# Kernel optimization log

Hardware: AMD Instinct MI355X
Metric: run time of the kernel (lower is better)

Reference implementation:

```python
import jax, jax.numpy as jnp
import numpy as np

N = 1048576
HID = 64
GEO = 15


def _glorot(key, in_dim, out_dim):
    # torch nn.Linear default init: U(-1/sqrt(in), 1/sqrt(in)); stored here as [in, out]
    bound = 1.0 / np.sqrt(in_dim)
    return jax.random.uniform(key, (in_dim, out_dim), jnp.float32, -bound, bound)


def setup_inputs() -> dict:
    key = jax.random.key(0)
    ks = jax.random.split(key, 8)
    x = jax.random.normal(ks[0], (N, 6), dtype=jnp.float32)
    # sigma_net: 3 -> 64 -> 64 -> (1 + geo_feat_dim)=16, no bias
    ws0 = _glorot(ks[1], 3, HID)
    ws1 = _glorot(ks[2], HID, HID)
    ws2 = _glorot(ks[3], HID, 1 + GEO)
    # color_net: (3 + 15)=18 -> 64 -> 64 -> 3, no bias
    wc0 = _glorot(ks[4], 3 + GEO, HID)
    wc1 = _glorot(ks[5], HID, HID)
    wc2 = _glorot(ks[6], HID, HID)
    wc3 = _glorot(ks[7], HID, 3)
    return {"x": x, "ws0": ws0, "ws1": ws1, "ws2": ws2,
            "wc0": wc0, "wc1": wc1, "wc2": wc2, "wc3": wc3}


def reference(x, ws0, ws1, ws2, wc0, wc1, wc2, wc3):
    input_pts, input_views = x[..., :3], x[..., 3:]
    # sigma net: Linear+ReLU x2, final Linear
    h = jax.nn.relu(input_pts @ ws0)
    h = jax.nn.relu(h @ ws1)
    h = h @ ws2                       # [N, 16]
    sigma = jax.nn.softplus(h[..., 0])  # [N]
    geo_feat = h[..., 1:]               # [N, 15]
    # color net
    c = jnp.concatenate([input_views, geo_feat], axis=-1)  # [N, 18]
    c = jax.nn.relu(c @ wc0)
    c = jax.nn.relu(c @ wc1)
    c = jax.nn.relu(c @ wc2)
    color = c @ wc3                    # [N, 3]
    return jnp.concatenate([color, sigma[..., None]], axis=-1)  # [N, 4]
```

## Files before the change

### kernel.cpp

```cpp
#include <hip/hip_runtime.h>
#include <math.h>
#include <stdint.h>

typedef short bf16x8 __attribute__((ext_vector_type(8)));
typedef float f32x4 __attribute__((ext_vector_type(4)));

#define NFRAGS 36
#define T 3
#define NW 4
#define BS 256
#define PTS_BLK (NW * T * 16)

__device__ __forceinline__ uint32_t f2bf_rne(float f) {
    uint32_t u = __float_as_uint(f);
    return (u + 0x7FFFu + ((u >> 16) & 1u)) >> 16;
}

__device__ __forceinline__ uint32_t pk2(float a, float b) {
    return __builtin_amdgcn_perm(__float_as_uint(b), __float_as_uint(a), 0x07060302u);
}
__device__ __forceinline__ uint32_t relu2(uint32_t x) {
    uint32_t r;
    asm("v_pk_max_i16 %0, %1, 0" : "=v"(r) : "v"(x));
    return r;
}
__device__ __forceinline__ uint32_t pk2r(float a, float b) { return relu2(pk2(a, b)); }
__device__ __forceinline__ uint16_t bfu(float v) { return (uint16_t)(__float_as_uint(v) >> 16); }

__device__ __forceinline__ int sperm(int k) {
    return (k & 3) | (((k >> 2) & 3) << 4) | (((k >> 4) & 3) << 2);
}
__device__ __forceinline__ int rperm(int k) {
    return (k & 32) | (((k >> 3) & 1) << 4) | (((k >> 4) & 1) << 3) | (k & 7);
}

__global__ void pack_weights(const float* __restrict__ ws0, const float* __restrict__ ws1,
                             const float* __restrict__ ws2, const float* __restrict__ wc0,
                             const float* __restrict__ wc1, const float* __restrict__ wc2,
                             const float* __restrict__ wc3, uint4* __restrict__ wpack) {
    int idx = blockIdx.x * blockDim.x + threadIdx.x;
    if (idx >= NFRAGS * 64) return;
    int F = idx >> 6, cl = idx & 63, cm = cl & 15, cq = cl >> 4;
    const float* w; int IN, OUT, mt, ks, pm;
    if (F < 4)       { w = ws0; IN = 3;  OUT = 64; mt = F;            ks = 0;          pm = 0; }
    else if (F < 12) { w = ws1; IN = 64; OUT = 64; mt = (F-4) >> 1;   ks = (F-4) & 1;  pm = 2; }
    else if (F < 14) { w = ws2; IN = 64; OUT = 16; mt = 0;            ks = F - 12;     pm = 2; }
    else if (F < 18) { w = wc0; IN = 18; OUT = 64; mt = F - 14;       ks = 0;          pm = 0; }
    else if (F < 26) { w = wc1; IN = 64; OUT = 64; mt = (F-18) >> 1;  ks = (F-18) & 1; pm = 2; }
    else if (F < 34) { w = wc2; IN = 64; OUT = 64; mt = (F-26) >> 1;  ks = (F-26) & 1; pm = 2; }
    else             { w = wc3; IN = 64; OUT = 3;  mt = 0;            ks = F - 34;     pm = 2; }
    const int fo = mt * 16 + cm;
    uint32_t pk[4];
    for (int jj = 0; jj < 4; ++jj) {
        uint32_t h[2];
        for (int bb = 0; bb < 2; ++bb) {
            int kg = ks * 32 + cq * 8 + jj * 2 + bb;
            int kr = (pm == 2) ? sperm(rperm(kg)) : kg;
            float v = 0.f;
            if (fo < OUT && kr < IN) v = w[kr * OUT + fo];
            h[bb] = f2bf_rne(v);
        }
        pk[jj] = h[0] | (h[1] << 16);
    }
    wpack[F * 64 + cl] = make_uint4(pk[0], pk[1], pk[2], pk[3]);
}

__global__ __launch_bounds__(BS, 4) void nerf_main(const float* __restrict__ xin,
                                                   const uint4* __restrict__ wpack,
                                                   float* __restrict__ outp, int n) {
    __shared__ __align__(16) char smem[NW * T * 2048];
    const int tid = threadIdx.x, wv = tid >> 6, lane = tid & 63;
    const int p = lane & 15, q = lane >> 4;
    const int sw = p & 7;
    char* actw = smem + wv * (T * 2048);
    const int base = blockIdx.x * PTS_BLK + wv * (T * 16);

    auto aaddr = [&](int t, int g) -> char* {
        return actw + t * 2048 + p * 128 + ((g ^ sw) << 4);
    };
    auto ldA = [&](int F) -> bf16x8 {
        uint4 u = wpack[F * 64 + lane];
        return *(bf16x8*)&u;
    };
    const f32x4 z4 = {0.f, 0.f, 0.f, 0.f};

    auto xpose = [&](const f32x4* d, bf16x8& b0, bf16x8& b1) {
        uint32_t X0 = pk2r(d[0][0], d[0][1]), X1 = pk2r(d[0][2], d[0][3]);
        uint32_t X2 = pk2r(d[1][0], d[1][1]), X3 = pk2r(d[1][2], d[1][3]);
        uint32_t X4 = pk2r(d[2][0], d[2][1]), X5 = pk2r(d[2][2], d[2][3]);
        uint32_t X6 = pk2r(d[3][0], d[3][1]), X7 = pk2r(d[3][2], d[3][3]);
        asm("v_permlane32_swap_b32 %0, %1" : "+v"(X0), "+v"(X4));
        asm("v_permlane32_swap_b32 %0, %1" : "+v"(X1), "+v"(X5));
        asm("v_permlane32_swap_b32 %0, %1" : "+v"(X2), "+v"(X6));
        asm("v_permlane32_swap_b32 %0, %1" : "+v"(X3), "+v"(X7));
        uint4 u0 = make_uint4(X0, X1, X2, X3), u1 = make_uint4(X4, X5, X6, X7);
        b0 = *(bf16x8*)&u0; b1 = *(bf16x8*)&u1;
    };

    float x0 = 0.f, x1 = 0.f, x2 = 0.f;
    float vv0 = 0.f, vv1 = 0.f, vv2 = 0.f;
    {
        const int pi = base + q * 16 + p;
        if (q < T && pi < n) {
            const float2* xp = (const float2*)(xin + (size_t)pi * 6);
            float2 a = xp[0], b = xp[1], c = xp[2];
            x0 = a.x; x1 = a.y; x2 = b.x; vv0 = b.y; vv1 = c.x; vv2 = c.y;
        }
    }

    bf16x8 W0[4];
#pragma unroll
    for (int i = 0; i < 4; ++i) W0[i] = ldA(i);
    bf16x8 W1[8];
#pragma unroll
    for (int i = 0; i < 8; ++i) W1[i] = ldA(4 + i);

    if (q < T) {
        *(uint4*)aaddr(q, 0) = make_uint4(pk2(x0, x1), pk2(x2, 0.f), 0u, 0u);
        *(uint4*)aaddr(q, 1) = make_uint4(0u, 0u, 0u, 0u);
        *(uint4*)aaddr(q, 2) = make_uint4(0u, 0u, 0u, 0u);
        *(uint4*)aaddr(q, 3) = make_uint4(0u, 0u, 0u, 0u);
    }

    bf16x8 c0[T], c1[T];

    auto layerK32 = [&](const bf16x8 (&W)[4]) {
#pragma unroll
        for (int t = 0; t < T; ++t) {
            bf16x8 b = *(const bf16x8*)aaddr(t, q);
            f32x4 d[4];
#pragma unroll
            for (int mt = 0; mt < 4; ++mt)
                d[mt] = __builtin_amdgcn_mfma_f32_16x16x32_bf16(W[mt], b, z4, 0, 0, 0);
            xpose(d, c0[t], c1[t]);
        }
    };

    auto layer64 = [&](const bf16x8 (&W)[8]) {
#pragma unroll
        for (int t = 0; t < T; ++t) {
            f32x4 d[4];
#pragma unroll
            for (int mt = 0; mt < 4; ++mt) {
                f32x4 acc = __builtin_amdgcn_mfma_f32_16x16x32_bf16(W[mt*2],   c0[t], z4,  0, 0, 0);
                d[mt]     = __builtin_amdgcn_mfma_f32_16x16x32_bf16(W[mt*2+1], c1[t], acc, 0, 0, 0);
            }
            xpose(d, c0[t], c1[t]);
        }
    };

    layerK32(W0);

    bf16x8 W2[2];
    W2[0] = ldA(12); W2[1] = ldA(13);

    layer64(W1);

    bf16x8 W3[4];
#pragma unroll
    for (int i = 0; i < 4; ++i) W3[i] = ldA(14 + i);

    float sig[T];
    {
#pragma unroll
        for (int t = 0; t < T; ++t) {
            f32x4 acc = __builtin_amdgcn_mfma_f32_16x16x32_bf16(W2[0], c0[t], z4,  0, 0, 0);
            f32x4 d   = __builtin_amdgcn_mfma_f32_16x16x32_bf16(W2[1], c1[t], acc, 0, 0, 0);
            const float sx = d[0];
            sig[t] = fmaxf(sx, 0.f) + __logf(1.f + __expf(-fabsf(sx)));
            *(uint4*)aaddr(t, q) = make_uint4(0u, 0u, 0u, 0u);
            if (q == t) {
                *(uint32_t*)(aaddr(t, 0) + 0) = pk2(vv0, vv1);
                *(uint16_t*)(aaddr(t, 0) + 4) = bfu(vv2);
            }
            if (q == 0) {
                *(uint16_t*)(aaddr(t, 0) + 6) = bfu(d[1]);
                *(uint32_t*)(aaddr(t, 0) + 8) = pk2(d[2], d[3]);
            } else if (q == 1) {
                *(uint32_t*)(aaddr(t, 0) + 12) = pk2(d[0], d[1]);
                *(uint32_t*)(aaddr(t, 1) + 0)  = pk2(d[2], d[3]);
            } else if (q == 2) {
                *(uint32_t*)(aaddr(t, 1) + 4) = pk2(d[0], d[1]);
                *(uint32_t*)(aaddr(t, 1) + 8) = pk2(d[2], d[3]);
            } else {
                *(uint32_t*)(aaddr(t, 1) + 12) = pk2(d[0], d[1]);
                *(uint32_t*)(aaddr(t, 2) + 0)  = pk2(d[2], d[3]);
            }
        }
    }

    bf16x8 W4[8];
#pragma unroll
    for (int i = 0; i < 8; ++i) W4[i] = ldA(18 + i);

    layerK32(W3);

    bf16x8 W5[8];
#pragma unroll
    for (int i = 0; i < 8; ++i) W5[i] = ldA(26 + i);

    layer64(W4);

    bf16x8 W6[2];
    W6[0] = ldA(34); W6[1] = ldA(35);

    layer64(W5);

    {
#pragma unroll
        for (int t = 0; t < T; ++t) {
            f32x4 acc = __builtin_amdgcn_mfma_f32_16x16x32_bf16(W6[0], c0[t], z4,  0, 0, 0);
            f32x4 d   = __builtin_amdgcn_mfma_f32_16x16x32_bf16(W6[1], c1[t], acc, 0, 0, 0);
            if (q == 0) {
                const int pt = base + t * 16 + p;
                if (pt < n)
                    *(float4*)(outp + (size_t)pt * 4) = make_float4(d[0], d[1], d[2], sig[t]);
            }
        }
    }
}

extern "C" void kernel_launch(void* const* d_in, const int* in_sizes, int n_in,
                              void* d_out, int out_size, void* d_ws, size_t ws_size,
                              hipStream_t stream) {
    const float* x   = (const float*)d_in[0];
    const float* ws0 = (const float*)d_in[1];
    const float* ws1 = (const float*)d_in[2];
    const float* ws2 = (const float*)d_in[3];
    const float* wc0 = (const float*)d_in[4];
    const float* wc1 = (const float*)d_in[5];
    const float* wc2 = (const float*)d_in[6];
    const float* wc3 = (const float*)d_in[7];
    float* out = (float*)d_out;
    uint4* wpack = (uint4*)d_ws;

    const int n = in_sizes[0] / 6;
    pack_weights<<<(NFRAGS * 64 + 255) / 256, 256, 0, stream>>>(ws0, ws1, ws2, wc0, wc1, wc2, wc3, wpack);
    const int grid = (n + PTS_BLK - 1) / PTS_BLK;
    nerf_main<<<grid, BS, 0, stream>>>(x, wpack, out, n);
}
```

Measured before the change: 116.1 us.

## Use persistent blocks with LDS-resident weights and prefetch of next chunk inputs

Measured after the change: 125.4 us. 8.0% more time.

```diff
diff --git a/kernel.cpp b/kernel.cpp
--- a/kernel.cpp
+++ b/kernel.cpp
@@ -6,10 +6,13 @@
 typedef float f32x4 __attribute__((ext_vector_type(4)));
 
 #define NFRAGS 36
-#define T 3
+#define T 4
 #define NW 4
 #define BS 256
 #define PTS_BLK (NW * T * 16)
+#define WBYTES (NFRAGS * 1024)
+#define ABYTES (NW * T * 1024)
+#define GRID_P 768
 
 __device__ __forceinline__ uint32_t f2bf_rne(float f) {
     uint32_t u = __float_as_uint(f);
@@ -67,20 +70,28 @@
 
 __global__ __launch_bounds__(BS, 4) void nerf_main(const float* __restrict__ xin,
                                                    const uint4* __restrict__ wpack,
-                                                   float* __restrict__ outp, int n) {
-    __shared__ __align__(16) char smem[NW * T * 2048];
+                                                   float* __restrict__ outp,
+                                                   int n, int nchunks) {
+    __shared__ __align__(16) char smem[WBYTES + ABYTES];
     const int tid = threadIdx.x, wv = tid >> 6, lane = tid & 63;
     const int p = lane & 15, q = lane >> 4;
-    const int sw = p & 7;
-    char* actw = smem + wv * (T * 2048);
-    const int base = blockIdx.x * PTS_BLK + wv * (T * 16);
-
+
+    {
+        uint4* wl = (uint4*)smem;
+        const uint4* __restrict__ ws = wpack;
+#pragma unroll
+        for (int i = 0; i < (NFRAGS * 64) / BS; ++i)
+            wl[tid + i * BS] = ws[tid + i * BS];
+    }
+
+    char* wbase = smem + lane * 16;
+    auto ldW = [&](int F) -> bf16x8 {
+        return *(const bf16x8*)(wbase + F * 1024);
+    };
+
+    char* actp = smem + WBYTES + wv * (T * 1024) + p * 64;
     auto aaddr = [&](int t, int g) -> char* {
-        return actw + t * 2048 + p * 128 + ((g ^ sw) << 4);
-    };
-    auto ldA = [&](int F) -> bf16x8 {
-        uint4 u = wpack[F * 64 + lane];
-        return *(bf16x8*)&u;
+        return actp + t * 1024 + (((g ^ (p & 3))) << 4);
     };
     const f32x4 z4 = {0.f, 0.f, 0.f, 0.f};
 
@@ -97,126 +108,123 @@
         b0 = *(bf16x8*)&u0; b1 = *(bf16x8*)&u1;
     };
 
-    float x0 = 0.f, x1 = 0.f, x2 = 0.f;
-    float vv0 = 0.f, vv1 = 0.f, vv2 = 0.f;
-    {
-        const int pi = base + q * 16 + p;
-        if (q < T && pi < n) {
+    bf16x8 c0[T], c1[T];
+
+    auto layerK32 = [&](int FB) {
+        bf16x8 W0 = ldW(FB), W1 = ldW(FB + 1), W2 = ldW(FB + 2), W3 = ldW(FB + 3);
+#pragma unroll
+        for (int t = 0; t < T; ++t) {
+            bf16x8 b = *(const bf16x8*)aaddr(t, q);
+            f32x4 d[4];
+            d[0] = __builtin_amdgcn_mfma_f32_16x16x32_bf16(W0, b, z4, 0, 0, 0);
+            d[1] = __builtin_amdgcn_mfma_f32_16x16x32_bf16(W1, b, z4, 0, 0, 0);
+            d[2] = __builtin_amdgcn_mfma_f32_16x16x32_bf16(W2, b, z4, 0, 0, 0);
+            d[3] = __builtin_amdgcn_mfma_f32_16x16x32_bf16(W3, b, z4, 0, 0, 0);
+            xpose(d, c0[t], c1[t]);
+        }
+    };
+
+    auto layer64 = [&](int FB) {
+        bf16x8 W[8];
+#pragma unroll
+        for (int i = 0; i < 8; ++i) W[i] = ldW(FB + i);
+#pragma unroll
+        for (int t = 0; t < T; ++t) {
+            f32x4 d[4];
+#pragma unroll
+            for (int mt = 0; mt < 4; ++mt) {
+                f32x4 acc = __builtin_amdgcn_mfma_f32_16x16x32_bf16(W[mt*2],   c0[t], z4,  0, 0, 0);
+                d[mt]     = __builtin_amdgcn_mfma_f32_16x16x32_bf16(W[mt*2+1], c1[t], acc, 0, 0, 0);
+            }
+            xpose(d, c0[t], c1[t]);
+        }
+    };
+
+    int chunk = blockIdx.x;
+    float2 xa = {0.f, 0.f}, xb = {0.f, 0.f}, xc = {0.f, 0.f};
+    if (chunk < nchunks) {
+        const int pi = chunk * PTS_BLK + wv * (T * 16) + q * 16 + p;
+        if (pi < n) {
             const float2* xp = (const float2*)(xin + (size_t)pi * 6);
-            float2 a = xp[0], b = xp[1], c = xp[2];
-            x0 = a.x; x1 = a.y; x2 = b.x; vv0 = b.y; vv1 = c.x; vv2 = c.y;
-        }
-    }
-
-    bf16x8 W0[4];
-#pragma unroll
-    for (int i = 0; i < 4; ++i) W0[i] = ldA(i);
-    bf16x8 W1[8];
-#pragma unroll
-    for (int i = 0; i < 8; ++i) W1[i] = ldA(4 + i);
-
-    if (q < T) {
-        *(uint4*)aaddr(q, 0) = make_uint4(pk2(x0, x1), pk2(x2, 0.f), 0u, 0u);
+            xa = xp[0]; xb = xp[1]; xc = xp[2];
+        }
+    }
+
+    __syncthreads();
+
+    for (; chunk < nchunks; chunk += gridDim.x) {
+        const int base = chunk * PTS_BLK + wv * (T * 16);
+        const float vv0 = xb.y, vv1 = xc.x, vv2 = xc.y;
+
+        *(uint4*)aaddr(q, 0) = make_uint4(pk2(xa.x, xa.y), pk2(xb.x, 0.f), 0u, 0u);
         *(uint4*)aaddr(q, 1) = make_uint4(0u, 0u, 0u, 0u);
         *(uint4*)aaddr(q, 2) = make_uint4(0u, 0u, 0u, 0u);
         *(uint4*)aaddr(q, 3) = make_uint4(0u, 0u, 0u, 0u);
-    }
-
-    bf16x8 c0[T], c1[T];
-
-    auto layerK32 = [&](const bf16x8 (&W)[4]) {
-#pragma unroll
-        for (int t = 0; t < T; ++t) {
-            bf16x8 b = *(const bf16x8*)aaddr(t, q);
-            f32x4 d[4];
-#pragma unroll
-            for (int mt = 0; mt < 4; ++mt)
-                d[mt] = __builtin_amdgcn_mfma_f32_16x16x32_bf16(W[mt], b, z4, 0, 0, 0);
-            xpose(d, c0[t], c1[t]);
-        }
-    };
-
-    auto layer64 = [&](const bf16x8 (&W)[8]) {
-#pragma unroll
-        for (int t = 0; t < T; ++t) {
-            f32x4 d[4];
-#pragma unroll
-            for (int mt = 0; mt < 4; ++mt) {
-                f32x4 acc = __builtin_amdgcn_mfma_f32_16x16x32_bf16(W[mt*2],   c0[t], z4,  0, 0, 0);
-                d[mt]     = __builtin_amdgcn_mfma_f32_16x16x32_bf16(W[mt*2+1], c1[t], acc, 0, 0, 0);
-            }
-            xpose(d, c0[t], c1[t]);
-        }
-    };
-
-    layerK32(W0);
-
-    bf16x8 W2[2];
-    W2[0] = ldA(12); W2[1] = ldA(13);
-
-    layer64(W1);
-
-    bf16x8 W3[4];
-#pragma unroll
-    for (int i = 0; i < 4; ++i) W3[i] = ldA(14 + i);
-
-    float sig[T];
-    {
-#pragma unroll
-        for (int t = 0; t < T; ++t) {
-            f32x4 acc = __builtin_amdgcn_mfma_f32_16x16x32_bf16(W2[0], c0[t], z4,  0, 0, 0);
-            f32x4 d   = __builtin_amdgcn_mfma_f32_16x16x32_bf16(W2[1], c1[t], acc, 0, 0, 0);
-            const float sx = d[0];
-            sig[t] = fmaxf(sx, 0.f) + __logf(1.f + __expf(-fabsf(sx)));
-            *(uint4*)aaddr(t, q) = make_uint4(0u, 0u, 0u, 0u);
-            if (q == t) {
-                *(uint32_t*)(aaddr(t, 0) + 0) = pk2(vv0, vv1);
-                *(uint16_t*)(aaddr(t, 0) + 4) = bfu(vv2);
-            }
-            if (q == 0) {
-                *(uint16_t*)(aaddr(t, 0) + 6) = bfu(d[1]);
-                *(uint32_t*)(aaddr(t, 0) + 8) = pk2(d[2], d[3]);
-            } else if (q == 1) {
-                *(uint32_t*)(aaddr(t, 0) + 12) = pk2(d[0], d[1]);
-                *(uint32_t*)(aaddr(t, 1) + 0)  = pk2(d[2], d[3]);
-            } else if (q == 2) {
-                *(uint32_t*)(aaddr(t, 1) + 4) = pk2(d[0], d[1]);
-                *(uint32_t*)(aaddr(t, 1) + 8) = pk2(d[2], d[3]);
-            } else {
-                *(uint32_t*)(aaddr(t, 1) + 12) = pk2(d[0], d[1]);
-                *(uint32_t*)(aaddr(t, 2) + 0)  = pk2(d[2], d[3]);
-            }
-        }
-    }
-
-    bf16x8 W4[8];
-#pragma unroll
-    for (int i = 0; i < 8; ++i) W4[i] = ldA(18 + i);
-
-    layerK32(W3);
-
-    bf16x8 W5[8];
-#pragma unroll
-    for (int i = 0; i < 8; ++i) W5[i] = ldA(26 + i);
-
-    layer64(W4);
-
-    bf16x8 W6[2];
-    W6[0] = ldA(34); W6[1] = ldA(35);
-
-    layer64(W5);
-
-    {
-#pragma unroll
-        for (int t = 0; t < T; ++t) {
-            f32x4 acc = __builtin_amdgcn_mfma_f32_16x16x32_bf16(W6[0], c0[t], z4,  0, 0, 0);
-            f32x4 d   = __builtin_amdgcn_mfma_f32_16x16x32_bf16(W6[1], c1[t], acc, 0, 0, 0);
-            if (q == 0) {
-                const int pt = base + t * 16 + p;
-                if (pt < n)
-                    *(float4*)(outp + (size_t)pt * 4) = make_float4(d[0], d[1], d[2], sig[t]);
-            }
-        }
+
+        const int nc = chunk + gridDim.x;
+        float2 na = {0.f, 0.f}, nb = {0.f, 0.f}, ncv = {0.f, 0.f};
+        if (nc < nchunks) {
+            const int pi2 = nc * PTS_BLK + wv * (T * 16) + q * 16 + p;
+            if (pi2 < n) {
+                const float2* xp2 = (const float2*)(xin + (size_t)pi2 * 6);
+                na = xp2[0]; nb = xp2[1]; ncv = xp2[2];
+            }
+        }
+
+        layerK32(0);
+
+        layer64(4);
+
+        float sig[T];
+        {
+            bf16x8 A0 = ldW(12), A1 = ldW(13);
+#pragma unroll
+            for (int t = 0; t < T; ++t) {
+                f32x4 acc = __builtin_amdgcn_mfma_f32_16x16x32_bf16(A0, c0[t], z4,  0, 0, 0);
+                f32x4 d   = __builtin_amdgcn_mfma_f32_16x16x32_bf16(A1, c1[t], acc, 0, 0, 0);
+                const float sx = d[0];
+                sig[t] = fmaxf(sx, 0.f) + __logf(1.f + __expf(-fabsf(sx)));
+                *(uint4*)aaddr(t, q) = make_uint4(0u, 0u, 0u, 0u);
+                if (q == t) {
+                    *(uint32_t*)(aaddr(t, 0) + 0) = pk2(vv0, vv1);
+                    *(uint16_t*)(aaddr(t, 0) + 4) = bfu(vv2);
+                }
+                if (q == 0) {
+                    *(uint16_t*)(aaddr(t, 0) + 6) = bfu(d[1]);
+                    *(uint32_t*)(aaddr(t, 0) + 8) = pk2(d[2], d[3]);
+                } else if (q == 1) {
+                    *(uint32_t*)(aaddr(t, 0) + 12) = pk2(d[0], d[1]);
+                    *(uint32_t*)(aaddr(t, 1) + 0)  = pk2(d[2], d[3]);
+                } else if (q == 2) {
+                    *(uint32_t*)(aaddr(t, 1) + 4) = pk2(d[0], d[1]);
+                    *(uint32_t*)(aaddr(t, 1) + 8) = pk2(d[2], d[3]);
+                } else {
+                    *(uint32_t*)(aaddr(t, 1) + 12) = pk2(d[0], d[1]);
+                    *(uint32_t*)(aaddr(t, 2) + 0)  = pk2(d[2], d[3]);
+                }
+            }
+        }
+
+        layerK32(14);
+
+        layer64(18);
+        layer64(26);
+
+        {
+            bf16x8 A0 = ldW(34), A1 = ldW(35);
+#pragma unroll
+            for (int t = 0; t < T; ++t) {
+                f32x4 acc = __builtin_amdgcn_mfma_f32_16x16x32_bf16(A0, c0[t], z4,  0, 0, 0);
+                f32x4 d   = __builtin_amdgcn_mfma_f32_16x16x32_bf16(A1, c1[t], acc, 0, 0, 0);
+                if (q == 0) {
+                    const int pt = base + t * 16 + p;
+                    if (pt < n)
+                        *(float4*)(outp + (size_t)pt * 4) = make_float4(d[0], d[1], d[2], sig[t]);
+                }
+            }
+        }
+
+        xa = na; xb = nb; xc = ncv;
     }
 }
 
@@ -236,6 +244,7 @@
 
     const int n = in_sizes[0] / 6;
     pack_weights<<<(NFRAGS * 64 + 255) / 256, 256, 0, stream>>>(ws0, ws1, ws2, wc0, wc1, wc2, wc3, wpack);
-    const int grid = (n + PTS_BLK - 1) / PTS_BLK;
-    nerf_main<<<grid, BS, 0, stream>>>(x, wpack, out, n);
-}
+    const int nchunks = (n + PTS_BLK - 1) / PTS_BLK;
+    const int grid = nchunks < GRID_P ? nchunks : GRID_P;
+    nerf_main<<<grid, BS, 0, stream>>>(x, wpack, out, n, nchunks);
+}
```

## Raise per-wave point tiles to four, load weights inside layers, add setprio

Applied to the files above, without the earlier changes.

Measured after the change: 116.4 us. Within noise of the previous version (+0.2%).

```diff
diff --git a/kernel.cpp b/kernel.cpp
--- a/kernel.cpp
+++ b/kernel.cpp
@@ -6,7 +6,7 @@
 typedef float f32x4 __attribute__((ext_vector_type(4)));
 
 #define NFRAGS 36
-#define T 3
+#define T 4
 #define NW 4
 #define BS 256
 #define PTS_BLK (NW * T * 16)
@@ -97,25 +97,15 @@
         b0 = *(bf16x8*)&u0; b1 = *(bf16x8*)&u1;
     };
 
-    float x0 = 0.f, x1 = 0.f, x2 = 0.f;
     float vv0 = 0.f, vv1 = 0.f, vv2 = 0.f;
     {
+        float x0 = 0.f, x1 = 0.f, x2 = 0.f;
         const int pi = base + q * 16 + p;
-        if (q < T && pi < n) {
+        if (pi < n) {
             const float2* xp = (const float2*)(xin + (size_t)pi * 6);
             float2 a = xp[0], b = xp[1], c = xp[2];
             x0 = a.x; x1 = a.y; x2 = b.x; vv0 = b.y; vv1 = c.x; vv2 = c.y;
         }
-    }
-
-    bf16x8 W0[4];
-#pragma unroll
-    for (int i = 0; i < 4; ++i) W0[i] = ldA(i);
-    bf16x8 W1[8];
-#pragma unroll
-    for (int i = 0; i < 8; ++i) W1[i] = ldA(4 + i);
-
-    if (q < T) {
         *(uint4*)aaddr(q, 0) = make_uint4(pk2(x0, x1), pk2(x2, 0.f), 0u, 0u);
         *(uint4*)aaddr(q, 1) = make_uint4(0u, 0u, 0u, 0u);
         *(uint4*)aaddr(q, 2) = make_uint4(0u, 0u, 0u, 0u);
@@ -124,48 +114,49 @@
 
     bf16x8 c0[T], c1[T];
 
-    auto layerK32 = [&](const bf16x8 (&W)[4]) {
+    auto layerK32 = [&](int FB) {
+        bf16x8 W0 = ldA(FB), W1 = ldA(FB + 1), W2 = ldA(FB + 2), W3 = ldA(FB + 3);
 #pragma unroll
         for (int t = 0; t < T; ++t) {
             bf16x8 b = *(const bf16x8*)aaddr(t, q);
             f32x4 d[4];
-#pragma unroll
-            for (int mt = 0; mt < 4; ++mt)
-                d[mt] = __builtin_amdgcn_mfma_f32_16x16x32_bf16(W[mt], b, z4, 0, 0, 0);
+            d[0] = __builtin_amdgcn_mfma_f32_16x16x32_bf16(W0, b, z4, 0, 0, 0);
+            d[1] = __builtin_amdgcn_mfma_f32_16x16x32_bf16(W1, b, z4, 0, 0, 0);
+            d[2] = __builtin_amdgcn_mfma_f32_16x16x32_bf16(W2, b, z4, 0, 0, 0);
+            d[3] = __builtin_amdgcn_mfma_f32_16x16x32_bf16(W3, b, z4, 0, 0, 0);
             xpose(d, c0[t], c1[t]);
         }
     };
 
-    auto layer64 = [&](const bf16x8 (&W)[8]) {
+    auto layer64 = [&](int FB) {
+        bf16x8 W[8];
+#pragma unroll
+        for (int i = 0; i < 8; ++i) W[i] = ldA(FB + i);
 #pragma unroll
         for (int t = 0; t < T; ++t) {
             f32x4 d[4];
+            __builtin_amdgcn_s_setprio(1);
 #pragma unroll
             for (int mt = 0; mt < 4; ++mt) {
                 f32x4 acc = __builtin_amdgcn_mfma_f32_16x16x32_bf16(W[mt*2],   c0[t], z4,  0, 0, 0);
                 d[mt]     = __builtin_amdgcn_mfma_f32_16x16x32_bf16(W[mt*2+1], c1[t], acc, 0, 0, 0);
             }
+            __builtin_amdgcn_s_setprio(0);
             xpose(d, c0[t], c1[t]);
         }
     };
 
-    layerK32(W0);
-
-    bf16x8 W2[2];
-    W2[0] = ldA(12); W2[1] = ldA(13);
-
-    layer64(W1);
-
-    bf16x8 W3[4];
-#pragma unroll
-    for (int i = 0; i < 4; ++i) W3[i] = ldA(14 + i);
+    layerK32(0);
+
+    layer64(4);
 
     float sig[T];
     {
-#pragma unroll
-        for (int t = 0; t < T; ++t) {
-            f32x4 acc = __builtin_amdgcn_mfma_f32_16x16x32_bf16(W2[0], c0[t], z4,  0, 0, 0);
-            f32x4 d   = __builtin_amdgcn_mfma_f32_16x16x32_bf16(W2[1], c1[t], acc, 0, 0, 0);
+        bf16x8 A0 = ldA(12), A1 = ldA(13);
+#pragma unroll
+        for (int t = 0; t < T; ++t) {
+            f32x4 acc = __builtin_amdgcn_mfma_f32_16x16x32_bf16(A0, c0[t], z4,  0, 0, 0);
+            f32x4 d   = __builtin_amdgcn_mfma_f32_16x16x32_bf16(A1, c1[t], acc, 0, 0, 0);
             const float sx = d[0];
             sig[t] = fmaxf(sx, 0.f) + __logf(1.f + __expf(-fabsf(sx)));
             *(uint4*)aaddr(t, q) = make_uint4(0u, 0u, 0u, 0u);
@@ -189,28 +180,17 @@
         }
     }
 
-    bf16x8 W4[8];
-#pragma unroll
-    for (int i = 0; i < 8; ++i) W4[i] = ldA(18 + i);
-
-    layerK32(W3);
-
-    bf16x8 W5[8];
-#pragma unroll
-    for (int i = 0; i < 8; ++i) W5[i] = ldA(26 + i);
-
-    layer64(W4);
-
-    bf16x8 W6[2];
-    W6[0] = ldA(34); W6[1] = ldA(35);
-
-    layer64(W5);
+    layerK32(14);
+
+    layer64(18);
+    layer64(26);
 
     {
-#pragma unroll
-        for (int t = 0; t < T; ++t) {
-            f32x4 acc = __builtin_amdgcn_mfma_f32_16x16x32_bf16(W6[0], c0[t], z4,  0, 0, 0);
-            f32x4 d   = __builtin_amdgcn_mfma_f32_16x16x32_bf16(W6[1], c1[t], acc, 0, 0, 0);
+        bf16x8 A0 = ldA(34), A1 = ldA(35);
+#pragma unroll
+        for (int t = 0; t < T; ++t) {
+            f32x4 acc = __builtin_amdgcn_mfma_f32_16x16x32_bf16(A0, c0[t], z4,  0, 0, 0);
+            f32x4 d   = __builtin_amdgcn_mfma_f32_16x16x32_bf16(A1, c1[t], acc, 0, 0, 0);
             if (q == 0) {
                 const int pt = base + t * 16 + p;
                 if (pt < n)
```
